# Kernel optimization log

Measured on AMD Instinct MI355X. Metric: run time of the kernel, lower is better.

Reference implementation:

```python
import jax, jax.numpy as jnp
import numpy as np

N = 50000   # num_nodes
E = 400000  # random edges (avg degree 8)


def setup_inputs() -> dict:
    key = jax.random.key(0)
    ks = jax.random.split(key, 12)

    def w(k, shape):
        # xavier-ish scaling
        return (jax.random.normal(k, shape, jnp.float32)
                / jnp.sqrt(jnp.float32(shape[0])))

    return {
        "node_emb": jax.random.normal(ks[0], (N, 128), jnp.float32) * 0.05,
        "edge_index": jax.random.randint(ks[1], (2, E), 0, N, dtype=jnp.int32),
        "W1": w(ks[2], (128, 512)), "b1": jnp.zeros((512,), jnp.float32),
        "W2": w(ks[3], (512, 128)), "b2": jnp.zeros((128,), jnp.float32),
        "Wres": w(ks[4], (512, 128)), "bres": jnp.zeros((128,), jnp.float32),
        "Wfc1": w(ks[5], (128, 256)), "bfc1": jnp.zeros((256,), jnp.float32),
        "Wfc2": w(ks[6], (256, 1)), "bfc2": jnp.zeros((1,), jnp.float32),
    }


def reference(node_emb, edge_index, W1, b1, W2, b2, Wres, bres,
              Wfc1, bfc1, Wfc2, bfc2):
    n = node_emb.shape[0]
    loops = jnp.arange(n, dtype=edge_index.dtype)
    # explicit add_self_loops in forward + GCNConv's internal gcn_norm self
    # loops => each node gets TWO self loops (faithful to the torch code).
    src = jnp.concatenate([edge_index[0], loops, loops])
    dst = jnp.concatenate([edge_index[1], loops, loops])

    deg = jax.ops.segment_sum(jnp.ones(src.shape, node_emb.dtype), dst,
                              num_segments=n)
    dinv = jnp.where(deg > 0, jax.lax.rsqrt(deg), 0.0)
    norm = dinv[src] * dinv[dst]  # [Etot]

    def gcn(x, W, b):
        h = x @ W                                    # [N, out]
        msg = h[src] * norm[:, None]                 # gather + scale
        agg = jax.ops.segment_sum(msg, dst, num_segments=n)  # scatter-add
        return agg + b

    x1 = jax.nn.relu(gcn(node_emb, W1, b1))   # [N, 512] (dropout = eval/id)
    x2 = jax.nn.relu(gcn(x1, W2, b2))          # [N, 128]
    x = x2 + x1 @ Wres + bres                  # residual projection
    A = jax.nn.relu(x @ Wfc1 + bfc1) @ Wfc2 + bfc2  # [N, 1]
    return (x, A)
```

## Files before the change

### kernel.cpp

```cpp
#include <hip/hip_runtime.h>


typedef unsigned short u16;
typedef short bf16x8 __attribute__((ext_vector_type(8)));
typedef unsigned short us8 __attribute__((ext_vector_type(8)));
typedef float f32x4 __attribute__((ext_vector_type(4)));

static inline int cdiv_ll(long long a, long long b) { return (int)((a + b - 1) / b); }

__device__ inline float bf2f(u16 u) {
    union { unsigned int i; float f; } v; v.i = ((unsigned int)u) << 16; return v.f;
}
__device__ inline u16 f2bf(float x) {
    union { float f; unsigned int i; } v; v.f = x;
    unsigned int r = v.i + 0x7fffu + ((v.i >> 16) & 1u);
    return (u16)(r >> 16);
}


__global__ __launch_bounds__(256) void zero_i32_kernel(int* __restrict__ p, int n) {
    int i = blockIdx.x * 256 + threadIdx.x;
    if (i < n) p[i] = 0;
}

__global__ __launch_bounds__(256) void hist_kernel(const int* __restrict__ dst,
                                                   int* __restrict__ cnt, int E) {
    int e = blockIdx.x * 256 + threadIdx.x;
    if (e < E) atomicAdd(&cnt[dst[e]], 1);
}

__global__ __launch_bounds__(256) void scanA_kernel(const int* __restrict__ cnt,
                                                    int* __restrict__ excl,
                                                    int* __restrict__ bsum, int N) {
    __shared__ int tmp[256];
    int i = blockIdx.x * 256 + threadIdx.x;
    int v = (i < N) ? cnt[i] : 0;
    tmp[threadIdx.x] = v;
    __syncthreads();
    for (int o = 1; o < 256; o <<= 1) {
        int t = (threadIdx.x >= (unsigned)o) ? tmp[threadIdx.x - o] : 0;
        __syncthreads();
        tmp[threadIdx.x] += t;
        __syncthreads();
    }
    if (i < N) excl[i] = tmp[threadIdx.x] - v;
    if (threadIdx.x == 255) bsum[blockIdx.x] = tmp[255];
}

__global__ __launch_bounds__(256) void scanB_kernel(int* __restrict__ bsum, int nb) {
    __shared__ int tmp[256];
    int v = (threadIdx.x < (unsigned)nb) ? bsum[threadIdx.x] : 0;
    tmp[threadIdx.x] = v;
    __syncthreads();
    for (int o = 1; o < 256; o <<= 1) {
        int t = (threadIdx.x >= (unsigned)o) ? tmp[threadIdx.x - o] : 0;
        __syncthreads();
        tmp[threadIdx.x] += t;
        __syncthreads();
    }
    if (threadIdx.x < (unsigned)nb) bsum[threadIdx.x] = tmp[threadIdx.x] - v;
}

__global__ __launch_bounds__(256) void scanC_kernel(const int* __restrict__ excl,
                                                    const int* __restrict__ bsum,
                                                    const int* __restrict__ cnt,
                                                    int* __restrict__ rowptr,
                                                    int* __restrict__ cursor,
                                                    float* __restrict__ dinv,
                                                    int N, int E) {
    int i = blockIdx.x * 256 + threadIdx.x;
    if (i < N) {
        int r = excl[i] + bsum[blockIdx.x];
        rowptr[i] = r;
        cursor[i] = r;
        dinv[i] = rsqrtf((float)cnt[i] + 2.0f);
    }
    if (i == 0) rowptr[N] = E;
}

__global__ __launch_bounds__(256) void fill_kernel(const int* __restrict__ src,
                                                   const int* __restrict__ dst,
                                                   const float* __restrict__ dinv,
                                                   int* __restrict__ cursor,
                                                   int* __restrict__ csr_src,
                                                   float* __restrict__ csr_w, int E) {
    int e = blockIdx.x * 256 + threadIdx.x;
    if (e >= E) return;
    int s = src[e], d = dst[e];
    int idx = atomicAdd(&cursor[d], 1);
    csr_src[idx] = s;
    csr_w[idx] = dinv[s] * dinv[d];
}


__global__ __launch_bounds__(256) void f2b_kernel(const float* __restrict__ x,
                                                  u16* __restrict__ y, long long n4) {
    long long tid = (long long)blockIdx.x * 256 + threadIdx.x;
    if (tid >= n4) return;
    float4 v = ((const float4*)x)[tid];
    uint2 o;
    o.x = (unsigned)f2bf(v.x) | ((unsigned)f2bf(v.y) << 16);
    o.y = (unsigned)f2bf(v.z) | ((unsigned)f2bf(v.w) << 16);
    ((uint2*)y)[tid] = o;
}

__global__ __launch_bounds__(256) void wtrans_kernel(const float* __restrict__ W,
                                                     u16* __restrict__ Wt, int K, int Nn) {
    int tid = blockIdx.x * 256 + threadIdx.x;
    if (tid >= K * Nn) return;
    int n = tid / K, k = tid % K;
    Wt[tid] = f2bf(W[(size_t)k * Nn + n]);
}

__global__ __launch_bounds__(256) void wcat_kernel(const float* __restrict__ W2,
                                                   const float* __restrict__ Wres,
                                                   u16* __restrict__ Wt, int K) {
    int tid = blockIdx.x * 256 + threadIdx.x;
    if (tid >= 256 * K) return;
    int n = tid / K, k = tid % K;
    float v = (n < 128) ? W2[(size_t)k * 128 + n] : Wres[(size_t)k * 128 + (n - 128)];
    Wt[tid] = f2bf(v);
}

__global__ __launch_bounds__(256) void initA_kernel(float* __restrict__ A,
                                                    const float* __restrict__ bfc2, int N) {
    int i = blockIdx.x * 256 + threadIdx.x;
    if (i < N) A[i] = bfc2[0];
}


__device__ inline void agg_row(const unsigned int* __restrict__ hp,
                               const int* __restrict__ rowptr,
                               const int* __restrict__ csr_src,
                               const float* __restrict__ csr_w,
                               const float* __restrict__ dinv,
                               int wid, int lane, float& ax, float& ay) {
    float dv = dinv[wid];
    unsigned int hv = hp[(size_t)wid * 64 + lane];
    float c0 = 2.0f * dv * dv;
    ax = bf2f((u16)hv) * c0;
    ay = bf2f((u16)(hv >> 16)) * c0;
    int e = rowptr[wid], e1 = rowptr[wid + 1];
    for (; e + 3 < e1; e += 4) {
        int s0 = csr_src[e], s1 = csr_src[e + 1], s2 = csr_src[e + 2], s3 = csr_src[e + 3];
        float w0 = csr_w[e], w1 = csr_w[e + 1], w2 = csr_w[e + 2], w3 = csr_w[e + 3];
        unsigned int v0 = hp[(size_t)s0 * 64 + lane];
        unsigned int v1 = hp[(size_t)s1 * 64 + lane];
        unsigned int v2 = hp[(size_t)s2 * 64 + lane];
        unsigned int v3 = hp[(size_t)s3 * 64 + lane];
        ax = fmaf(bf2f((u16)v0), w0, ax); ay = fmaf(bf2f((u16)(v0 >> 16)), w0, ay);
        ax = fmaf(bf2f((u16)v1), w1, ax); ay = fmaf(bf2f((u16)(v1 >> 16)), w1, ay);
        ax = fmaf(bf2f((u16)v2), w2, ax); ay = fmaf(bf2f((u16)(v2 >> 16)), w2, ay);
        ax = fmaf(bf2f((u16)v3), w3, ax); ay = fmaf(bf2f((u16)(v3 >> 16)), w3, ay);
    }
    for (; e < e1; ++e) {
        int s0 = csr_src[e]; float w0 = csr_w[e];
        unsigned int v0 = hp[(size_t)s0 * 64 + lane];
        ax = fmaf(bf2f((u16)v0), w0, ax); ay = fmaf(bf2f((u16)(v0 >> 16)), w0, ay);
    }
}

__global__ __launch_bounds__(256) void aggb_kernel(const u16* __restrict__ hb,
                                                   const int* __restrict__ rowptr,
                                                   const int* __restrict__ csr_src,
                                                   const float* __restrict__ csr_w,
                                                   const float* __restrict__ dinv,
                                                   u16* __restrict__ out, int N) {
    int wid  = (blockIdx.x * blockDim.x + threadIdx.x) >> 6;
    int lane = threadIdx.x & 63;
    if (wid >= N) return;
    float ax, ay;
    agg_row((const unsigned int*)hb, rowptr, csr_src, csr_w, dinv, wid, lane, ax, ay);
    ((unsigned int*)out)[(size_t)wid * 64 + lane] =
        (unsigned)f2bf(ax) | ((unsigned)f2bf(ay) << 16);
}

__global__ __launch_bounds__(256) void aggfin_kernel(const u16* __restrict__ hb,
                                                     const int* __restrict__ rowptr,
                                                     const int* __restrict__ csr_src,
                                                     const float* __restrict__ csr_w,
                                                     const float* __restrict__ dinv,
                                                     const float* __restrict__ b2,
                                                     const float* __restrict__ bres,
                                                     float* __restrict__ xout,
                                                     u16* __restrict__ xb, int N) {
    int wid  = (blockIdx.x * blockDim.x + threadIdx.x) >> 6;
    int lane = threadIdx.x & 63;
    if (wid >= N) return;
    float ax, ay;
    agg_row((const unsigned int*)hb, rowptr, csr_src, csr_w, dinv, wid, lane, ax, ay);
    float2 bb = ((const float2*)b2)[lane];
    float2 rr = ((const float2*)bres)[lane];
    float2 hres = ((float2*)xout)[(size_t)wid * 64 + lane];
    float ox = fmaxf(ax + bb.x, 0.f) + hres.x + rr.x;
    float oy = fmaxf(ay + bb.y, 0.f) + hres.y + rr.y;
    ((float2*)xout)[(size_t)wid * 64 + lane] = make_float2(ox, oy);
    ((unsigned int*)xb)[(size_t)wid * 64 + lane] =
        (unsigned)f2bf(ox) | ((unsigned)f2bf(oy) << 16);
}


template <int MODE>
__global__ __launch_bounds__(512) void mgemm(const u16* __restrict__ A,
                                             const u16* __restrict__ Bt,
                                             int M, int Nn, int K,
                                             const float* __restrict__ bias,
                                             u16* __restrict__ Cb,
                                             float* __restrict__ Cf,
                                             const float* __restrict__ w2) {
    __shared__ u16 As[128][72];
    __shared__ u16 Bs[256][72];
    const int t = threadIdx.x;
    const int bm = blockIdx.y * 128;
    const int bn = blockIdx.x * 256;
    const int w = t >> 6, lane = t & 63;
    const int wm = w >> 2, wn = w & 3;
    const int l15 = lane & 15, lg = lane >> 4;

    f32x4 acc[4][4];
#pragma unroll
    for (int i = 0; i < 4; ++i)
#pragma unroll
        for (int j = 0; j < 4; ++j) acc[i][j] = (f32x4)(0.0f);

    for (int kk = 0; kk < K; kk += 64) {
#pragma unroll
        for (int i = 0; i < 2; ++i) {
            int c = t + 512 * i;
            int row = c >> 3, cs = (c & 7) * 8;
            us8 v = (us8)(u16)0;
            if (bm + row < M)
                v = *(const us8*)(A + (size_t)(bm + row) * K + kk + cs);
            *(us8*)&As[row][cs] = v;
        }
#pragma unroll
        for (int i = 0; i < 4; ++i) {
            int c = t + 512 * i;
            int row = c >> 3, cs = (c & 7) * 8;
            us8 v = *(const us8*)(Bt + (size_t)(bn + row) * K + kk + cs);
            *(us8*)&Bs[row][cs] = v;
        }
        __syncthreads();
#pragma unroll
        for (int ks = 0; ks < 2; ++ks) {
            const int ko = 32 * ks + lg * 8;
            bf16x8 bfr[4], afr[4];
#pragma unroll
            for (int fn = 0; fn < 4; ++fn)
                bfr[fn] = *(const bf16x8*)&Bs[64 * wn + 16 * fn + l15][ko];
#pragma unroll
            for (int fm = 0; fm < 4; ++fm)
                afr[fm] = *(const bf16x8*)&As[64 * wm + 16 * fm + l15][ko];
#pragma unroll
            for (int fm = 0; fm < 4; ++fm)
#pragma unroll
                for (int fn = 0; fn < 4; ++fn)
                    acc[fm][fn] = __builtin_amdgcn_mfma_f32_16x16x32_bf16(
                        afr[fm], bfr[fn], acc[fm][fn], 0, 0, 0);
        }
        __syncthreads();
    }

    if (MODE == 3) {
        float bl[4], wl[4];
#pragma unroll
        for (int fn = 0; fn < 4; ++fn) {
            int col = bn + 64 * wn + 16 * fn + l15;
            bl[fn] = bias[col];
            wl[fn] = w2[col];
        }
#pragma unroll
        for (int fm = 0; fm < 4; ++fm) {
#pragma unroll
            for (int r = 0; r < 4; ++r) {
                int row = bm + 64 * wm + 16 * fm + lg * 4 + r;
                float p = 0.f;
#pragma unroll
                for (int fn = 0; fn < 4; ++fn)
                    p += fmaxf(acc[fm][fn][r] + bl[fn], 0.f) * wl[fn];
                p += __shfl_xor(p, 1);
                p += __shfl_xor(p, 2);
                p += __shfl_xor(p, 4);
                p += __shfl_xor(p, 8);
                if (l15 == 0 && row < M) atomicAdd(&Cf[row], p);
            }
        }
        return;
    }

#pragma unroll
    for (int fm = 0; fm < 4; ++fm) {
#pragma unroll
        for (int fn = 0; fn < 4; ++fn) {
            const int col = bn + 64 * wn + 16 * fn + l15;
#pragma unroll
            for (int r = 0; r < 4; ++r) {
                int row = bm + 64 * wm + 16 * fm + lg * 4 + r;
                if (row < M) {
                    float v = acc[fm][fn][r];
                    if (MODE == 1) {
                        v = fmaxf(v + bias[col], 0.0f);
                        Cb[(size_t)row * Nn + col] = f2bf(v);
                    } else {
                        if (col < 128) Cb[(size_t)row * 128 + col] = f2bf(v);
                        else           Cf[(size_t)row * 128 + (col - 128)] = v;
                    }
                }
            }
        }
    }
}


extern "C" void kernel_launch(void* const* d_in, const int* in_sizes, int n_in,
                              void* d_out, int out_size, void* d_ws, size_t ws_size,
                              hipStream_t stream) {
    const float* emb  = (const float*)d_in[0];
    const int*   eidx = (const int*)d_in[1];
    const float* W1   = (const float*)d_in[2];
    const float* b1   = (const float*)d_in[3];
    const float* W2   = (const float*)d_in[4];
    const float* b2   = (const float*)d_in[5];
    const float* Wres = (const float*)d_in[6];
    const float* bres = (const float*)d_in[7];
    const float* Wfc1 = (const float*)d_in[8];
    const float* bfc1 = (const float*)d_in[9];
    const float* Wfc2 = (const float*)d_in[10];
    const float* bfc2 = (const float*)d_in[11];

    const int N = in_sizes[0] / 128;
    const int E = in_sizes[1] / 2;
    const int* srcv = eidx;
    const int* dstv = eidx + E;

    float* out  = (float*)d_out;
    float* xout = out;
    float* Aout = out + (size_t)N * 128;

    char* p = (char*)d_ws;
    float* dinv  = (float*)p;            p += (size_t)N * 4;
    float* csr_w = (float*)p;            p += (size_t)E * 4;
    u16*  embb   = (u16*)p;              p += (size_t)N * 128 * 2;
    u16*  aggEb  = (u16*)p;              p += (size_t)N * 128 * 2;
    u16*  x1b    = (u16*)p;              p += (size_t)N * 512 * 2;
    u16*  h2b    = (u16*)p;              p += (size_t)N * 128 * 2;
    u16*  xb     = (u16*)p;              p += (size_t)N * 128 * 2;
    u16*  W1t    = (u16*)p;              p += (size_t)512 * 128 * 2;
    u16*  Wct    = (u16*)p;              p += (size_t)256 * 512 * 2;
    u16*  Wfc1t  = (u16*)p;              p += (size_t)256 * 128 * 2;
    int*  cnt     = (int*)p;             p += (size_t)N * 4;
    int*  excl    = (int*)p;             p += (size_t)N * 4;
    int*  rowptr  = (int*)p;             p += (size_t)(N + 1) * 4;
    int*  cursor  = (int*)p;             p += (size_t)N * 4;
    int*  bsum    = (int*)p;             p += 256 * 4;
    int*  csr_src = (int*)p;             p += (size_t)E * 4;

    const int T  = 256;
    const int nb = cdiv_ll(N, 256);

    zero_i32_kernel<<<cdiv_ll(N, T), T, 0, stream>>>(cnt, N);
    hist_kernel<<<cdiv_ll(E, T), T, 0, stream>>>(dstv, cnt, E);
    scanA_kernel<<<nb, T, 0, stream>>>(cnt, excl, bsum, N);
    scanB_kernel<<<1, T, 0, stream>>>(bsum, nb);
    scanC_kernel<<<nb, T, 0, stream>>>(excl, bsum, cnt, rowptr, cursor, dinv, N, E);
    fill_kernel<<<cdiv_ll(E, T), T, 0, stream>>>(srcv, dstv, dinv, cursor, csr_src, csr_w, E);

    f2b_kernel<<<cdiv_ll((long long)N * 32, T), T, 0, stream>>>(emb, embb, (long long)N * 32);
    wtrans_kernel<<<cdiv_ll(128 * 512, T), T, 0, stream>>>(W1, W1t, 128, 512);
    wcat_kernel<<<cdiv_ll(256 * 512, T), T, 0, stream>>>(W2, Wres, Wct, 512);
    wtrans_kernel<<<cdiv_ll(128 * 256, T), T, 0, stream>>>(Wfc1, Wfc1t, 128, 256);
    initA_kernel<<<cdiv_ll(N, T), T, 0, stream>>>(Aout, bfc2, N);

    aggb_kernel<<<cdiv_ll((long long)N * 64, T), T, 0, stream>>>(
        embb, rowptr, csr_src, csr_w, dinv, aggEb, N);

    mgemm<1><<<dim3(512 / 256, cdiv_ll(N, 128)), 512, 0, stream>>>(
        aggEb, W1t, N, 512, 128, b1, x1b, nullptr, nullptr);

    mgemm<2><<<dim3(1, cdiv_ll(N, 128)), 512, 0, stream>>>(
        x1b, Wct, N, 256, 512, nullptr, h2b, xout, nullptr);

    aggfin_kernel<<<cdiv_ll((long long)N * 64, T), T, 0, stream>>>(
        h2b, rowptr, csr_src, csr_w, dinv, b2, bres, xout, xb, N);

    mgemm<3><<<dim3(1, cdiv_ll(N, 128)), 512, 0, stream>>>(
        xb, Wfc1t, N, 256, 128, bfc1, nullptr, Aout, Wfc2);
}
```

Before: 215.6 us.

## Merge setup kernels, unroll edge aggregation by eight, prefetch GEMM tiles into registers

Five small preprocessing kernels (embedding bf16 conversion, three weight transposes, count zeroing, output init) are merged into one setup kernel to cut launch count. The CSR aggregation loop is unrolled to eight edges per iteration to keep more gathers in flight. The MFMA GEMM now loads the next K tile into registers while the current tile is being computed, software-pipelining global loads against LDS compute at the cost of more registers.

```diff
diff --git a/kernel.cpp b/kernel.cpp
--- a/kernel.cpp
+++ b/kernel.cpp
@@ -18,10 +18,54 @@
 }
 
 
-__global__ __launch_bounds__(256) void zero_i32_kernel(int* __restrict__ p, int n) {
-    int i = blockIdx.x * 256 + threadIdx.x;
-    if (i < n) p[i] = 0;
-}
+__global__ __launch_bounds__(256) void setup_kernel(const float* __restrict__ emb,
+                                                    const float* __restrict__ W1,
+                                                    const float* __restrict__ W2,
+                                                    const float* __restrict__ Wres,
+                                                    const float* __restrict__ Wfc1,
+                                                    const float* __restrict__ bfc2,
+                                                    u16* __restrict__ embb,
+                                                    u16* __restrict__ W1t,
+                                                    u16* __restrict__ Wct,
+                                                    u16* __restrict__ Wfc1t,
+                                                    int* __restrict__ cnt,
+                                                    float* __restrict__ Aout,
+                                                    int N) {
+    long long r = (long long)blockIdx.x * 256 + threadIdx.x;
+    const long long nf2b = (long long)N * 32;
+    if (r < nf2b) {
+        float4 v = ((const float4*)emb)[r];
+        uint2 o;
+        o.x = (unsigned)f2bf(v.x) | ((unsigned)f2bf(v.y) << 16);
+        o.y = (unsigned)f2bf(v.z) | ((unsigned)f2bf(v.w) << 16);
+        ((uint2*)embb)[r] = o;
+        return;
+    }
+    r -= nf2b;
+    if (r < 512 * 128) {
+        int n = (int)(r / 128), k = (int)(r % 128);
+        W1t[r] = f2bf(W1[(size_t)k * 512 + n]);
+        return;
+    }
+    r -= 512 * 128;
+    if (r < 256 * 512) {
+        int n = (int)(r / 512), k = (int)(r % 512);
+        float v = (n < 128) ? W2[(size_t)k * 128 + n] : Wres[(size_t)k * 128 + (n - 128)];
+        Wct[r] = f2bf(v);
+        return;
+    }
+    r -= 256 * 512;
+    if (r < 256 * 128) {
+        int n = (int)(r / 128), k = (int)(r % 128);
+        Wfc1t[r] = f2bf(Wfc1[(size_t)k * 256 + n]);
+        return;
+    }
+    r -= 256 * 128;
+    if (r < N) { cnt[(int)r] = 0; return; }
+    r -= N;
+    if (r < N) Aout[(int)r] = bfc2[0];
+}
+
 
 __global__ __launch_bounds__(256) void hist_kernel(const int* __restrict__ dst,
                                                    int* __restrict__ cnt, int E) {
@@ -93,41 +137,12 @@
 }
 
 
-__global__ __launch_bounds__(256) void f2b_kernel(const float* __restrict__ x,
-                                                  u16* __restrict__ y, long long n4) {
-    long long tid = (long long)blockIdx.x * 256 + threadIdx.x;
-    if (tid >= n4) return;
-    float4 v = ((const float4*)x)[tid];
-    uint2 o;
-    o.x = (unsigned)f2bf(v.x) | ((unsigned)f2bf(v.y) << 16);
-    o.y = (unsigned)f2bf(v.z) | ((unsigned)f2bf(v.w) << 16);
-    ((uint2*)y)[tid] = o;
-}
-
-__global__ __launch_bounds__(256) void wtrans_kernel(const float* __restrict__ W,
-                                                     u16* __restrict__ Wt, int K, int Nn) {
-    int tid = blockIdx.x * 256 + threadIdx.x;
-    if (tid >= K * Nn) return;
-    int n = tid / K, k = tid % K;
-    Wt[tid] = f2bf(W[(size_t)k * Nn + n]);
-}
-
-__global__ __launch_bounds__(256) void wcat_kernel(const float* __restrict__ W2,
-                                                   const float* __restrict__ Wres,
-                                                   u16* __restrict__ Wt, int K) {
-    int tid = blockIdx.x * 256 + threadIdx.x;
-    if (tid >= 256 * K) return;
-    int n = tid / K, k = tid % K;
-    float v = (n < 128) ? W2[(size_t)k * 128 + n] : Wres[(size_t)k * 128 + (n - 128)];
-    Wt[tid] = f2bf(v);
-}
-
-__global__ __launch_bounds__(256) void initA_kernel(float* __restrict__ A,
-                                                    const float* __restrict__ bfc2, int N) {
-    int i = blockIdx.x * 256 + threadIdx.x;
-    if (i < N) A[i] = bfc2[0];
-}
-
+#define AGG_EDGE(SR, WR)                                                       \
+    {                                                                          \
+        unsigned int vv = hp[(size_t)(SR) * 64 + lane];                        \
+        ax = fmaf(bf2f((u16)vv), (WR), ax);                                    \
+        ay = fmaf(bf2f((u16)(vv >> 16)), (WR), ay);                            \
+    }
 
 __device__ inline void agg_row(const unsigned int* __restrict__ hp,
                                const int* __restrict__ rowptr,
@@ -141,22 +156,23 @@
     ax = bf2f((u16)hv) * c0;
     ay = bf2f((u16)(hv >> 16)) * c0;
     int e = rowptr[wid], e1 = rowptr[wid + 1];
-    for (; e + 3 < e1; e += 4) {
-        int s0 = csr_src[e], s1 = csr_src[e + 1], s2 = csr_src[e + 2], s3 = csr_src[e + 3];
-        float w0 = csr_w[e], w1 = csr_w[e + 1], w2 = csr_w[e + 2], w3 = csr_w[e + 3];
-        unsigned int v0 = hp[(size_t)s0 * 64 + lane];
-        unsigned int v1 = hp[(size_t)s1 * 64 + lane];
-        unsigned int v2 = hp[(size_t)s2 * 64 + lane];
-        unsigned int v3 = hp[(size_t)s3 * 64 + lane];
-        ax = fmaf(bf2f((u16)v0), w0, ax); ay = fmaf(bf2f((u16)(v0 >> 16)), w0, ay);
-        ax = fmaf(bf2f((u16)v1), w1, ax); ay = fmaf(bf2f((u16)(v1 >> 16)), w1, ay);
-        ax = fmaf(bf2f((u16)v2), w2, ax); ay = fmaf(bf2f((u16)(v2 >> 16)), w2, ay);
-        ax = fmaf(bf2f((u16)v3), w3, ax); ay = fmaf(bf2f((u16)(v3 >> 16)), w3, ay);
+    for (; e + 7 < e1; e += 8) {
+        int s0 = csr_src[e + 0], s1 = csr_src[e + 1], s2 = csr_src[e + 2], s3 = csr_src[e + 3];
+        int s4 = csr_src[e + 4], s5 = csr_src[e + 5], s6 = csr_src[e + 6], s7 = csr_src[e + 7];
+        float w0 = csr_w[e + 0], w1 = csr_w[e + 1], w2 = csr_w[e + 2], w3 = csr_w[e + 3];
+        float w4 = csr_w[e + 4], w5 = csr_w[e + 5], w6 = csr_w[e + 6], w7 = csr_w[e + 7];
+        AGG_EDGE(s0, w0); AGG_EDGE(s1, w1); AGG_EDGE(s2, w2); AGG_EDGE(s3, w3);
+        AGG_EDGE(s4, w4); AGG_EDGE(s5, w5); AGG_EDGE(s6, w6); AGG_EDGE(s7, w7);
+    }
+    if (e + 3 < e1) {
+        int s0 = csr_src[e + 0], s1 = csr_src[e + 1], s2 = csr_src[e + 2], s3 = csr_src[e + 3];
+        float w0 = csr_w[e + 0], w1 = csr_w[e + 1], w2 = csr_w[e + 2], w3 = csr_w[e + 3];
+        AGG_EDGE(s0, w0); AGG_EDGE(s1, w1); AGG_EDGE(s2, w2); AGG_EDGE(s3, w3);
+        e += 4;
     }
     for (; e < e1; ++e) {
         int s0 = csr_src[e]; float w0 = csr_w[e];
-        unsigned int v0 = hp[(size_t)s0 * 64 + lane];
-        ax = fmaf(bf2f((u16)v0), w0, ax); ay = fmaf(bf2f((u16)(v0 >> 16)), w0, ay);
+        AGG_EDGE(s0, w0);
     }
 }
 
@@ -216,6 +232,7 @@
     const int w = t >> 6, lane = t & 63;
     const int wm = w >> 2, wn = w & 3;
     const int l15 = lane & 15, lg = lane >> 4;
+    const int srow = t >> 3, scol = (t & 7) * 8;
 
     f32x4 acc[4][4];
 #pragma unroll
@@ -223,24 +240,43 @@
 #pragma unroll
         for (int j = 0; j < 4; ++j) acc[i][j] = (f32x4)(0.0f);
 
+    us8 ra[2], rb[4];
+#pragma unroll
+    for (int i = 0; i < 2; ++i) {
+        int row = srow + 64 * i;
+        us8 v = (us8)(u16)0;
+        if (bm + row < M) v = *(const us8*)(A + (size_t)(bm + row) * K + scol);
+        ra[i] = v;
+    }
+#pragma unroll
+    for (int i = 0; i < 4; ++i) {
+        int row = srow + 64 * i;
+        rb[i] = *(const us8*)(Bt + (size_t)(bn + row) * K + scol);
+    }
+
     for (int kk = 0; kk < K; kk += 64) {
 #pragma unroll
-        for (int i = 0; i < 2; ++i) {
-            int c = t + 512 * i;
-            int row = c >> 3, cs = (c & 7) * 8;
-            us8 v = (us8)(u16)0;
-            if (bm + row < M)
-                v = *(const us8*)(A + (size_t)(bm + row) * K + kk + cs);
-            *(us8*)&As[row][cs] = v;
+        for (int i = 0; i < 2; ++i) *(us8*)&As[srow + 64 * i][scol] = ra[i];
+#pragma unroll
+        for (int i = 0; i < 4; ++i) *(us8*)&Bs[srow + 64 * i][scol] = rb[i];
+        __syncthreads();
+
+        if (kk + 64 < K) {
+#pragma unroll
+            for (int i = 0; i < 2; ++i) {
+                int row = srow + 64 * i;
+                us8 v = (us8)(u16)0;
+                if (bm + row < M)
+                    v = *(const us8*)(A + (size_t)(bm + row) * K + kk + 64 + scol);
+                ra[i] = v;
+            }
+#pragma unroll
+            for (int i = 0; i < 4; ++i) {
+                int row = srow + 64 * i;
+                rb[i] = *(const us8*)(Bt + (size_t)(bn + row) * K + kk + 64 + scol);
+            }
         }
-#pragma unroll
-        for (int i = 0; i < 4; ++i) {
-            int c = t + 512 * i;
-            int row = c >> 3, cs = (c & 7) * 8;
-            us8 v = *(const us8*)(Bt + (size_t)(bn + row) * K + kk + cs);
-            *(us8*)&Bs[row][cs] = v;
-        }
-        __syncthreads();
+
 #pragma unroll
         for (int ks = 0; ks < 2; ++ks) {
             const int ko = 32 * ks + lg * 8;
@@ -358,19 +394,17 @@
     const int T  = 256;
     const int nb = cdiv_ll(N, 256);
 
-    zero_i32_kernel<<<cdiv_ll(N, T), T, 0, stream>>>(cnt, N);
+    const long long setup_work = (long long)N * 32 + 512 * 128 + 256 * 512
+                               + 256 * 128 + (long long)N + (long long)N;
+    setup_kernel<<<cdiv_ll(setup_work, T), T, 0, stream>>>(
+        emb, W1, W2, Wres, Wfc1, bfc2, embb, W1t, Wct, Wfc1t, cnt, Aout, N);
+
     hist_kernel<<<cdiv_ll(E, T), T, 0, stream>>>(dstv, cnt, E);
     scanA_kernel<<<nb, T, 0, stream>>>(cnt, excl, bsum, N);
     scanB_kernel<<<1, T, 0, stream>>>(bsum, nb);
     scanC_kernel<<<nb, T, 0, stream>>>(excl, bsum, cnt, rowptr, cursor, dinv, N, E);
     fill_kernel<<<cdiv_ll(E, T), T, 0, stream>>>(srcv, dstv, dinv, cursor, csr_src, csr_w, E);
 
-    f2b_kernel<<<cdiv_ll((long long)N * 32, T), T, 0, stream>>>(emb, embb, (long long)N * 32);
-    wtrans_kernel<<<cdiv_ll(128 * 512, T), T, 0, stream>>>(W1, W1t, 128, 512);
-    wcat_kernel<<<cdiv_ll(256 * 512, T), T, 0, stream>>>(W2, Wres, Wct, 512);
-    wtrans_kernel<<<cdiv_ll(128 * 256, T), T, 0, stream>>>(Wfc1, Wfc1t, 128, 256);
-    initA_kernel<<<cdiv_ll(N, T), T, 0, stream>>>(Aout, bfc2, N);
-
     aggb_kernel<<<cdiv_ll((long long)N * 64, T), T, 0, stream>>>(
         embb, rowptr, csr_src, csr_w, dinv, aggEb, N);
 
```

Result: slower. 220.9 us (+2.4%).
